# Performance work log

Hardware: AMD Instinct MI355X
Metric: run time of the kernel (lower is better)

## Reference

```python
import jax, jax.numpy as jnp
import numpy as np

B, T, C, H = 128, 512, 128, 64  # batch, seq, n_embd, head_size


def setup_inputs() -> dict:
    key = jax.random.key(0)
    ks = jax.random.split(key, 6)
    s = 1.0 / np.sqrt(C)
    return {
        "x": jax.random.normal(ks[0], (B, T, C), dtype=jnp.float32),
        "Wg": jax.random.normal(ks[1], (C, C), dtype=jnp.float32) * s,
        "bg": jnp.zeros((C,), dtype=jnp.float32),
        "Wk": jax.random.normal(ks[2], (C, H), dtype=jnp.float32) * s,
        "Wq": jax.random.normal(ks[3], (C, H), dtype=jnp.float32) * s,
        "Wv": jax.random.normal(ks[4], (C, H), dtype=jnp.float32) * s,
    }


def reference(x, Wg, bg, Wk, Wq, Wv):
    # GateLayer: x * sigmoid(Linear(x))
    g = jax.nn.sigmoid(jnp.einsum('btc,cd->btd', x, Wg) + bg)
    xg = x * g
    k = jnp.einsum('btc,ch->bth', xg, Wk)
    q = jnp.einsum('btc,ch->bth', xg, Wq)
    v = jnp.einsum('btc,ch->bth', xg, Wv)
    # NOTE: original scales by C**-0.5 (n_embd), not head_size**-0.5
    scale = C ** -0.5
    wei = jnp.einsum('bqh,bkh->bqk', q, k) * scale  # [B,T,T]
    causal = jnp.tril(jnp.ones((T, T), dtype=bool))
    wei = jnp.where(causal, wei, -jnp.inf)
    wei = jax.nn.softmax(wei, axis=-1)
    # dropout is identity in eval mode
    out = jnp.einsum('bqk,bkh->bqh', wei, v)  # [B,T,H]
    return out
```

## Files before the change

### kernel.cpp

```cpp
#include <hip/hip_runtime.h>


#define BB 128
#define TB 512
#define CC 128
#define HH 64

static constexpr float SCALE = 0.088388347648318447f;

typedef __attribute__((ext_vector_type(8))) short bf16x8;
typedef __attribute__((ext_vector_type(8))) unsigned short u16x8;
typedef __attribute__((ext_vector_type(4))) float f32x4;

__device__ inline unsigned short f2bf(float f) {
    union { float f; unsigned u; } x; x.f = f;
    unsigned r = x.u + 0x7fff + ((x.u >> 16) & 1);
    return (unsigned short)(r >> 16);
}
__device__ inline float bf2f(unsigned short h) {
    union { unsigned u; float f; } x; x.u = ((unsigned)h) << 16;
    return x.f;
}
__device__ inline bf16x8 pack8(float4 a, float4 b) {
    bf16x8 o;
    o[0] = (short)f2bf(a.x); o[1] = (short)f2bf(a.y);
    o[2] = (short)f2bf(a.z); o[3] = (short)f2bf(a.w);
    o[4] = (short)f2bf(b.x); o[5] = (short)f2bf(b.y);
    o[6] = (short)f2bf(b.z); o[7] = (short)f2bf(b.w);
    return o;
}

__global__ void prep_weights(const float* __restrict__ Wg, const float* __restrict__ Wk,
                             const float* __restrict__ Wq, const float* __restrict__ Wv,
                             unsigned short* __restrict__ WgT, unsigned short* __restrict__ WkT,
                             unsigned short* __restrict__ WqT, unsigned short* __restrict__ WvT)
{
    int idx = blockIdx.x * 256 + threadIdx.x;
    if (idx < 16384) {
        int n = idx >> 7, k = idx & 127;
        WgT[idx] = f2bf(Wg[k * CC + n]);
    } else {
        int j = idx - 16384;
        int mtx = j >> 13;
        int r = j & 8191;
        int n = r >> 7, k = r & 127;
        const float* W = (mtx == 0) ? Wk : (mtx == 1) ? Wq : Wv;
        unsigned short* WT = (mtx == 0) ? WkT : (mtx == 1) ? WqT : WvT;
        WT[r] = f2bf(W[k * HH + n]);
    }
}

__global__ __launch_bounds__(256, 2) void gate_qkv_kernel(
    const float* __restrict__ x, const float* __restrict__ bg,
    const unsigned short* __restrict__ WgT, const unsigned short* __restrict__ WkT,
    const unsigned short* __restrict__ WqT, const unsigned short* __restrict__ WvT,
    unsigned short* __restrict__ qo, unsigned short* __restrict__ ko,
    unsigned short* __restrict__ vto)
{
    __shared__ unsigned short wlds[192 * 136];
    __shared__ unsigned short slice[4][32 * 40];

    const int tid  = threadIdx.x;
    const int wv   = tid >> 6;
    const int lane = tid & 63;
    const int l15  = lane & 15;
    const int quad = lane >> 4;
    const int R0   = blockIdx.x * 128;
    const int row0 = R0 + 32 * wv;

#pragma unroll
    for (int it = 0; it < 8; ++it) {
        int idx = tid + 256 * it;
        int r = idx >> 4, c8 = idx & 15;
        *(u16x8*)(wlds + r * 136 + c8 * 8) = *(const u16x8*)(WgT + r * 128 + c8 * 8);
    }

    bf16x8 bx[2][4];
#pragma unroll
    for (int mt = 0; mt < 2; ++mt)
#pragma unroll
        for (int kc = 0; kc < 4; ++kc) {
            const float* p = x + (size_t)(row0 + 16 * mt + l15) * CC + kc * 32 + quad * 8;
            float4 a = *(const float4*)p;
            float4 c = *(const float4*)(p + 4);
            bx[mt][kc] = pack8(a, c);
        }

    float4 xe[8][2];
#pragma unroll
    for (int nt = 0; nt < 8; ++nt)
#pragma unroll
        for (int mt = 0; mt < 2; ++mt)
            xe[nt][mt] = *(const float4*)(x + (size_t)(row0 + 16 * mt + l15) * CC +
                                          16 * nt + 4 * quad);

    __syncthreads();

    f32x4 acc[8][2];
#pragma unroll
    for (int nt = 0; nt < 8; ++nt)
#pragma unroll
        for (int mt = 0; mt < 2; ++mt) acc[nt][mt] = (f32x4){0.f, 0.f, 0.f, 0.f};

#pragma unroll
    for (int nt = 0; nt < 8; ++nt) {
#pragma unroll
        for (int kc = 0; kc < 4; ++kc) {
            bf16x8 aw = *(const bf16x8*)(wlds + (16 * nt + l15) * 136 + kc * 32 + quad * 8);
#pragma unroll
            for (int mt = 0; mt < 2; ++mt)
                acc[nt][mt] = __builtin_amdgcn_mfma_f32_16x16x32_bf16(
                    aw, bx[mt][kc], acc[nt][mt], 0, 0, 0);
        }
    }

    unsigned short* sl = slice[wv];
    bf16x8 bxg[2][4];
#pragma unroll
    for (int kc = 0; kc < 4; ++kc) {
#pragma unroll
        for (int half = 0; half < 2; ++half) {
            int nt = 2 * kc + half;
            float4 bgv = *(const float4*)(bg + 16 * nt + 4 * quad);
#pragma unroll
            for (int mt = 0; mt < 2; ++mt) {
                float e0 = __expf(-(acc[nt][mt][0] + bgv.x));
                float e1 = __expf(-(acc[nt][mt][1] + bgv.y));
                float e2 = __expf(-(acc[nt][mt][2] + bgv.z));
                float e3 = __expf(-(acc[nt][mt][3] + bgv.w));
                ushort4 o;
                o.x = f2bf(xe[nt][mt].x * __builtin_amdgcn_rcpf(1.f + e0));
                o.y = f2bf(xe[nt][mt].y * __builtin_amdgcn_rcpf(1.f + e1));
                o.z = f2bf(xe[nt][mt].z * __builtin_amdgcn_rcpf(1.f + e2));
                o.w = f2bf(xe[nt][mt].w * __builtin_amdgcn_rcpf(1.f + e3));
                *(ushort4*)(sl + (16 * mt + l15) * 40 + 16 * half + 4 * quad) = o;
            }
        }
#pragma unroll
        for (int mt = 0; mt < 2; ++mt)
            bxg[mt][kc] = *(const bf16x8*)(sl + (16 * mt + l15) * 40 + quad * 8);
    }

    __syncthreads();

#pragma unroll
    for (int it = 0; it < 12; ++it) {
        int idx = tid + 256 * it;
        int r = idx >> 4, c8 = idx & 15;
        const unsigned short* src = (r < 64) ? (WkT + r * 128)
                                  : (r < 128) ? (WqT + (r - 64) * 128)
                                              : (WvT + (r - 128) * 128);
        *(u16x8*)(wlds + r * 136 + c8 * 8) = *(const u16x8*)(src + c8 * 8);
    }
    __syncthreads();

    const int b = R0 >> 9, t0 = R0 & 511;
#pragma unroll
    for (int pj = 0; pj < 3; ++pj) {
        f32x4 pacc[4][2];
#pragma unroll
        for (int nt = 0; nt < 4; ++nt)
#pragma unroll
            for (int mt = 0; mt < 2; ++mt) pacc[nt][mt] = (f32x4){0.f, 0.f, 0.f, 0.f};

#pragma unroll
        for (int nt = 0; nt < 4; ++nt) {
#pragma unroll
            for (int kc = 0; kc < 4; ++kc) {
                bf16x8 aw = *(const bf16x8*)(wlds + (64 * pj + 16 * nt + l15) * 136 +
                                             kc * 32 + quad * 8);
#pragma unroll
                for (int mt = 0; mt < 2; ++mt)
                    pacc[nt][mt] = __builtin_amdgcn_mfma_f32_16x16x32_bf16(
                        aw, bxg[mt][kc], pacc[nt][mt], 0, 0, 0);
            }
        }

        if (pj < 2) {
            unsigned short* O = (pj == 0) ? ko : qo;
#pragma unroll
            for (int nt = 0; nt < 4; ++nt)
#pragma unroll
                for (int mt = 0; mt < 2; ++mt) {
                    int m = 32 * wv + 16 * mt + l15;
                    ushort4 h;
                    h.x = f2bf(pacc[nt][mt][0]); h.y = f2bf(pacc[nt][mt][1]);
                    h.z = f2bf(pacc[nt][mt][2]); h.w = f2bf(pacc[nt][mt][3]);
                    *(ushort4*)(O + (size_t)(R0 + m) * HH + 16 * nt + quad * 4) = h;
                }
        } else {
#pragma unroll
            for (int nt = 0; nt < 4; ++nt)
#pragma unroll
                for (int mt = 0; mt < 2; ++mt) {
                    int m = 32 * wv + 16 * mt + l15;
                    unsigned short* dst =
                        vto + (size_t)b * (HH * TB) + (16 * nt + quad * 4) * TB + t0 + m;
#pragma unroll
                    for (int r = 0; r < 4; ++r)
                        dst[r * TB] = f2bf(pacc[nt][mt][r]);
                }
        }
    }
}

__device__ __forceinline__ void pv_nomax(const f32x4* s, f32x4& lacc, f32x4* o4,
                                         unsigned short* ps, const bf16x8* bv0,
                                         const bf16x8* bv1, const bf16x8 ones,
                                         int wave, int l15, int quad)
{
#pragma unroll
    for (int nt = 0; nt < 4; ++nt)
#pragma unroll
        for (int r = 0; r < 4; ++r)
            ps[(16 * wave + quad * 4 + r) * 76 + 16 * nt + l15] = f2bf(__expf(s[nt][r]));

    bf16x8 ap0 = *(const bf16x8*)(ps + (16 * wave + l15) * 76 + quad * 8);
    bf16x8 ap1 = *(const bf16x8*)(ps + (16 * wave + l15) * 76 + 32 + quad * 8);
    lacc = __builtin_amdgcn_mfma_f32_16x16x32_bf16(ap0, ones, lacc, 0, 0, 0);
    lacc = __builtin_amdgcn_mfma_f32_16x16x32_bf16(ap1, ones, lacc, 0, 0, 0);
#pragma unroll
    for (int nt = 0; nt < 4; ++nt) {
        o4[nt] = __builtin_amdgcn_mfma_f32_16x16x32_bf16(ap0, bv0[nt], o4[nt], 0, 0, 0);
        o4[nt] = __builtin_amdgcn_mfma_f32_16x16x32_bf16(ap1, bv1[nt], o4[nt], 0, 0, 0);
    }
}

__device__ __forceinline__ void attn_epilogue(const f32x4* o4, const f32x4 lacc,
                                              float* out, size_t base, int q0,
                                              int wave, int l15, int quad)
{
    float inv[4];
#pragma unroll
    for (int r = 0; r < 4; ++r) inv[r] = __builtin_amdgcn_rcpf(lacc[r]);
#pragma unroll
    for (int nt = 0; nt < 4; ++nt)
#pragma unroll
        for (int r = 0; r < 4; ++r)
            out[base + (size_t)(q0 + 16 * wave + quad * 4 + r) * HH + 16 * nt + l15] =
                o4[nt][r] * inv[r];
}

__global__ __launch_bounds__(256, 2) void attn_kernel(
    const unsigned short* __restrict__ q, const unsigned short* __restrict__ k,
    const unsigned short* __restrict__ vt, float* __restrict__ out)
{
    __shared__ unsigned short ks[64 * 72];
    __shared__ unsigned short vs[64 * 72];
    __shared__ unsigned short ps[64 * 76];

    const int tid  = threadIdx.x;
    const int wave = tid >> 6;
    const int lane = tid & 63;
    const int l15  = lane & 15;
    const int quad = lane >> 4;
    const int pr   = blockIdx.x;
    const int b    = blockIdx.y;
    const size_t base = (size_t)b * TB * HH;

    const int qtA = pr, qtB = 7 - pr;
    const int q0A = qtA * 64, q0B = qtB * 64;

    bf16x8 ones;
#pragma unroll
    for (int i = 0; i < 8; ++i) ones[i] = (short)0x3F80;

    const int r0 = tid >> 3, c8 = (tid & 7) * 8;
    const int r1 = r0 + 32;

    bf16x8 kr0 = *(const bf16x8*)(k + base + (size_t)r0 * HH + c8);
    bf16x8 kr1 = *(const bf16x8*)(k + base + (size_t)r1 * HH + c8);
    bf16x8 vr0 = *(const bf16x8*)(vt + base + (size_t)r0 * TB + c8);
    bf16x8 vr1 = *(const bf16x8*)(vt + base + (size_t)r1 * TB + c8);

    const unsigned short* qrA = q + base + (size_t)(q0A + 16 * wave + l15) * HH;
    const unsigned short* qrB = q + base + (size_t)(q0B + 16 * wave + l15) * HH;
    bf16x8 aqA0 = *(const bf16x8*)(qrA + quad * 8);
    bf16x8 aqA1 = *(const bf16x8*)(qrA + 32 + quad * 8);
    bf16x8 aqB0 = *(const bf16x8*)(qrB + quad * 8);
    bf16x8 aqB1 = *(const bf16x8*)(qrB + 32 + quad * 8);

    f32x4 oA[4], oB[4], lAacc, lBacc;
#pragma unroll
    for (int nt = 0; nt < 4; ++nt) {
        oA[nt] = (f32x4){0.f, 0.f, 0.f, 0.f};
        oB[nt] = (f32x4){0.f, 0.f, 0.f, 0.f};
    }
    lAacc = (f32x4){0.f, 0.f, 0.f, 0.f};
    lBacc = (f32x4){0.f, 0.f, 0.f, 0.f};

    const int nIt = qtB + 1;
    for (int kt = 0; kt < nIt; ++kt) {
        __syncthreads();
        *(bf16x8*)(ks + r0 * 72 + c8) = kr0;
        *(bf16x8*)(ks + r1 * 72 + c8) = kr1;
        *(bf16x8*)(vs + r0 * 72 + c8) = vr0;
        *(bf16x8*)(vs + r1 * 72 + c8) = vr1;
        __syncthreads();

        if (kt + 1 < nIt) {
            const int k0n = (kt + 1) * 64;
            kr0 = *(const bf16x8*)(k + base + (size_t)(k0n + r0) * HH + c8);
            kr1 = *(const bf16x8*)(k + base + (size_t)(k0n + r1) * HH + c8);
            vr0 = *(const bf16x8*)(vt + base + (size_t)r0 * TB + k0n + c8);
            vr1 = *(const bf16x8*)(vt + base + (size_t)r1 * TB + k0n + c8);
        }

        bf16x8 bk0[4], bk1[4], bv0[4], bv1[4];
#pragma unroll
        for (int nt = 0; nt < 4; ++nt) {
            bk0[nt] = *(const bf16x8*)(ks + (16 * nt + l15) * 72 + quad * 8);
            bk1[nt] = *(const bf16x8*)(ks + (16 * nt + l15) * 72 + 32 + quad * 8);
            bv0[nt] = *(const bf16x8*)(vs + (16 * nt + l15) * 72 + quad * 8);
            bv1[nt] = *(const bf16x8*)(vs + (16 * nt + l15) * 72 + 32 + quad * 8);
        }

        const bool actA = (kt <= qtA);

        f32x4 sA[4], sB[4];
#pragma unroll
        for (int nt = 0; nt < 4; ++nt) {
            f32x4 zb = (f32x4){0.f, 0.f, 0.f, 0.f};
            zb = __builtin_amdgcn_mfma_f32_16x16x32_bf16(aqB0, bk0[nt], zb, 0, 0, 0);
            zb = __builtin_amdgcn_mfma_f32_16x16x32_bf16(aqB1, bk1[nt], zb, 0, 0, 0);
            sB[nt] = zb;
            if (actA) {
                f32x4 za = (f32x4){0.f, 0.f, 0.f, 0.f};
                za = __builtin_amdgcn_mfma_f32_16x16x32_bf16(aqA0, bk0[nt], za, 0, 0, 0);
                za = __builtin_amdgcn_mfma_f32_16x16x32_bf16(aqA1, bk1[nt], za, 0, 0, 0);
                sA[nt] = za;
            }
        }

        if (actA) {
            const bool diagA = (kt == qtA);
#pragma unroll
            for (int nt = 0; nt < 4; ++nt)
#pragma unroll
                for (int r = 0; r < 4; ++r) {
                    float sv = sA[nt][r] * SCALE;
                    if (diagA && (16 * nt + l15) > (16 * wave + quad * 4 + r)) sv = -1e30f;
                    sA[nt][r] = sv;
                }
            pv_nomax(sA, lAacc, oA, ps, bv0, bv1, ones, wave, l15, quad);
            if (diagA) attn_epilogue(oA, lAacc, out, base, q0A, wave, l15, quad);
        }

        {
            const bool diagB = (kt == qtB);
#pragma unroll
            for (int nt = 0; nt < 4; ++nt)
#pragma unroll
                for (int r = 0; r < 4; ++r) {
                    float sv = sB[nt][r] * SCALE;
                    if (diagB && (16 * nt + l15) > (16 * wave + quad * 4 + r)) sv = -1e30f;
                    sB[nt][r] = sv;
                }
            pv_nomax(sB, lBacc, oB, ps, bv0, bv1, ones, wave, l15, quad);
        }
    }

    attn_epilogue(oB, lBacc, out, base, q0B, wave, l15, quad);
}

extern "C" void kernel_launch(void* const* d_in, const int* in_sizes, int n_in,
                              void* d_out, int out_size, void* d_ws, size_t ws_size,
                              hipStream_t stream) {
    const float* x  = (const float*)d_in[0];
    const float* Wg = (const float*)d_in[1];
    const float* bg = (const float*)d_in[2];
    const float* Wk = (const float*)d_in[3];
    const float* Wq = (const float*)d_in[4];
    const float* Wv = (const float*)d_in[5];
    float* out = (float*)d_out;

    unsigned short* ws = (unsigned short*)d_ws;
    const size_t BTH = (size_t)BB * TB * HH;
    unsigned short* qo  = ws;
    unsigned short* ko  = ws + BTH;
    unsigned short* vto = ws + 2 * BTH;
    unsigned short* WgT = ws + 3 * BTH;
    unsigned short* WkT = WgT + 16384;
    unsigned short* WqT = WkT + 8192;
    unsigned short* WvT = WqT + 8192;

    hipLaunchKernelGGL(prep_weights, dim3(160), dim3(256), 0, stream,
                       Wg, Wk, Wq, Wv, WgT, WkT, WqT, WvT);
    hipLaunchKernelGGL(gate_qkv_kernel, dim3(BB * TB / 128), dim3(256), 0, stream,
                       x, bg, WgT, WkT, WqT, WvT, qo, ko, vto);
    hipLaunchKernelGGL(attn_kernel, dim3(4, BB), dim3(256), 0, stream,
                       qo, ko, vto, out);
}
```

Measured before the change: 120.8 us.

## Split paired query tiles into one block per tile with transposed score MFMA

Each attention block previously handled two query tiles (qt and 7-qt) to balance causal work. Now each block handles a single query tile, the grid becomes (B, 8) with the longest tiles scheduled first, and launch bounds allow three blocks per CU. The score MFMA operands are swapped so each lane holds a row of P and can write four contiguous bf16 values, and exp is computed with exp2f using a pre-multiplied log2e scale. This trades the per-block load balancing for more blocks and occupancy, and the K/V tiles that were shared between the two query tiles are now reloaded by separate blocks.

```diff
diff --git a/kernel.cpp b/kernel.cpp
--- a/kernel.cpp
+++ b/kernel.cpp
@@ -6,7 +6,8 @@
 #define CC 128
 #define HH 64
 
-static constexpr float SCALE = 0.088388347648318447f;
+static constexpr float SEXP2 =
+    (float)(0.088388347648318447 * 1.4426950408889634);
 
 typedef __attribute__((ext_vector_type(8))) short bf16x8;
 typedef __attribute__((ext_vector_type(8))) unsigned short u16x8;
@@ -16,10 +17,6 @@
     union { float f; unsigned u; } x; x.f = f;
     unsigned r = x.u + 0x7fff + ((x.u >> 16) & 1);
     return (unsigned short)(r >> 16);
-}
-__device__ inline float bf2f(unsigned short h) {
-    union { unsigned u; float f; } x; x.u = ((unsigned)h) << 16;
-    return x.f;
 }
 __device__ inline bf16x8 pack8(float4 a, float4 b) {
     bf16x8 o;
@@ -204,44 +201,7 @@
     }
 }
 
-__device__ __forceinline__ void pv_nomax(const f32x4* s, f32x4& lacc, f32x4* o4,
-                                         unsigned short* ps, const bf16x8* bv0,
-                                         const bf16x8* bv1, const bf16x8 ones,
-                                         int wave, int l15, int quad)
-{
-#pragma unroll
-    for (int nt = 0; nt < 4; ++nt)
-#pragma unroll
-        for (int r = 0; r < 4; ++r)
-            ps[(16 * wave + quad * 4 + r) * 76 + 16 * nt + l15] = f2bf(__expf(s[nt][r]));
-
-    bf16x8 ap0 = *(const bf16x8*)(ps + (16 * wave + l15) * 76 + quad * 8);
-    bf16x8 ap1 = *(const bf16x8*)(ps + (16 * wave + l15) * 76 + 32 + quad * 8);
-    lacc = __builtin_amdgcn_mfma_f32_16x16x32_bf16(ap0, ones, lacc, 0, 0, 0);
-    lacc = __builtin_amdgcn_mfma_f32_16x16x32_bf16(ap1, ones, lacc, 0, 0, 0);
-#pragma unroll
-    for (int nt = 0; nt < 4; ++nt) {
-        o4[nt] = __builtin_amdgcn_mfma_f32_16x16x32_bf16(ap0, bv0[nt], o4[nt], 0, 0, 0);
-        o4[nt] = __builtin_amdgcn_mfma_f32_16x16x32_bf16(ap1, bv1[nt], o4[nt], 0, 0, 0);
-    }
-}
-
-__device__ __forceinline__ void attn_epilogue(const f32x4* o4, const f32x4 lacc,
-                                              float* out, size_t base, int q0,
-                                              int wave, int l15, int quad)
-{
-    float inv[4];
-#pragma unroll
-    for (int r = 0; r < 4; ++r) inv[r] = __builtin_amdgcn_rcpf(lacc[r]);
-#pragma unroll
-    for (int nt = 0; nt < 4; ++nt)
-#pragma unroll
-        for (int r = 0; r < 4; ++r)
-            out[base + (size_t)(q0 + 16 * wave + quad * 4 + r) * HH + 16 * nt + l15] =
-                o4[nt][r] * inv[r];
-}
-
-__global__ __launch_bounds__(256, 2) void attn_kernel(
+__global__ __launch_bounds__(256, 3) void attn_kernel(
     const unsigned short* __restrict__ q, const unsigned short* __restrict__ k,
     const unsigned short* __restrict__ vt, float* __restrict__ out)
 {
@@ -254,12 +214,10 @@
     const int lane = tid & 63;
     const int l15  = lane & 15;
     const int quad = lane >> 4;
-    const int pr   = blockIdx.x;
-    const int b    = blockIdx.y;
+    const int b    = blockIdx.x;
+    const int qt   = 7 - blockIdx.y;
+    const int q0   = qt * 64;
     const size_t base = (size_t)b * TB * HH;
-
-    const int qtA = pr, qtB = 7 - pr;
-    const int q0A = qtA * 64, q0B = qtB * 64;
 
     bf16x8 ones;
 #pragma unroll
@@ -273,23 +231,16 @@
     bf16x8 vr0 = *(const bf16x8*)(vt + base + (size_t)r0 * TB + c8);
     bf16x8 vr1 = *(const bf16x8*)(vt + base + (size_t)r1 * TB + c8);
 
-    const unsigned short* qrA = q + base + (size_t)(q0A + 16 * wave + l15) * HH;
-    const unsigned short* qrB = q + base + (size_t)(q0B + 16 * wave + l15) * HH;
-    bf16x8 aqA0 = *(const bf16x8*)(qrA + quad * 8);
-    bf16x8 aqA1 = *(const bf16x8*)(qrA + 32 + quad * 8);
-    bf16x8 aqB0 = *(const bf16x8*)(qrB + quad * 8);
-    bf16x8 aqB1 = *(const bf16x8*)(qrB + 32 + quad * 8);
-
-    f32x4 oA[4], oB[4], lAacc, lBacc;
-#pragma unroll
-    for (int nt = 0; nt < 4; ++nt) {
-        oA[nt] = (f32x4){0.f, 0.f, 0.f, 0.f};
-        oB[nt] = (f32x4){0.f, 0.f, 0.f, 0.f};
-    }
-    lAacc = (f32x4){0.f, 0.f, 0.f, 0.f};
-    lBacc = (f32x4){0.f, 0.f, 0.f, 0.f};
-
-    const int nIt = qtB + 1;
+    const unsigned short* qr = q + base + (size_t)(q0 + 16 * wave + l15) * HH;
+    bf16x8 aq0 = *(const bf16x8*)(qr + quad * 8);
+    bf16x8 aq1 = *(const bf16x8*)(qr + 32 + quad * 8);
+
+    f32x4 o[4], lacc;
+#pragma unroll
+    for (int nt = 0; nt < 4; ++nt) o[nt] = (f32x4){0.f, 0.f, 0.f, 0.f};
+    lacc = (f32x4){0.f, 0.f, 0.f, 0.f};
+
+    const int nIt = qt + 1;
     for (int kt = 0; kt < nIt; ++kt) {
         __syncthreads();
         *(bf16x8*)(ks + r0 * 72 + c8) = kr0;
@@ -315,52 +266,51 @@
             bv1[nt] = *(const bf16x8*)(vs + (16 * nt + l15) * 72 + 32 + quad * 8);
         }
 
-        const bool actA = (kt <= qtA);
-
-        f32x4 sA[4], sB[4];
-#pragma unroll
-        for (int nt = 0; nt < 4; ++nt) {
-            f32x4 zb = (f32x4){0.f, 0.f, 0.f, 0.f};
-            zb = __builtin_amdgcn_mfma_f32_16x16x32_bf16(aqB0, bk0[nt], zb, 0, 0, 0);
-            zb = __builtin_amdgcn_mfma_f32_16x16x32_bf16(aqB1, bk1[nt], zb, 0, 0, 0);
-            sB[nt] = zb;
-            if (actA) {
-                f32x4 za = (f32x4){0.f, 0.f, 0.f, 0.f};
-                za = __builtin_amdgcn_mfma_f32_16x16x32_bf16(aqA0, bk0[nt], za, 0, 0, 0);
-                za = __builtin_amdgcn_mfma_f32_16x16x32_bf16(aqA1, bk1[nt], za, 0, 0, 0);
-                sA[nt] = za;
+        f32x4 s[4];
+#pragma unroll
+        for (int nt = 0; nt < 4; ++nt) {
+            f32x4 z = (f32x4){0.f, 0.f, 0.f, 0.f};
+            z = __builtin_amdgcn_mfma_f32_16x16x32_bf16(bk0[nt], aq0, z, 0, 0, 0);
+            z = __builtin_amdgcn_mfma_f32_16x16x32_bf16(bk1[nt], aq1, z, 0, 0, 0);
+            s[nt] = z;
+        }
+
+        const bool diag = (kt == qt);
+        unsigned short* pr = ps + (16 * wave + l15) * 76;
+#pragma unroll
+        for (int nt = 0; nt < 4; ++nt) {
+            float p[4];
+#pragma unroll
+            for (int r = 0; r < 4; ++r) {
+                float sv = s[nt][r] * SEXP2;
+                if (diag && (16 * nt + 4 * quad + r) > (16 * wave + l15)) sv = -1e30f;
+                p[r] = exp2f(sv);
             }
-        }
-
-        if (actA) {
-            const bool diagA = (kt == qtA);
-#pragma unroll
-            for (int nt = 0; nt < 4; ++nt)
-#pragma unroll
-                for (int r = 0; r < 4; ++r) {
-                    float sv = sA[nt][r] * SCALE;
-                    if (diagA && (16 * nt + l15) > (16 * wave + quad * 4 + r)) sv = -1e30f;
-                    sA[nt][r] = sv;
-                }
-            pv_nomax(sA, lAacc, oA, ps, bv0, bv1, ones, wave, l15, quad);
-            if (diagA) attn_epilogue(oA, lAacc, out, base, q0A, wave, l15, quad);
-        }
-
-        {
-            const bool diagB = (kt == qtB);
-#pragma unroll
-            for (int nt = 0; nt < 4; ++nt)
-#pragma unroll
-                for (int r = 0; r < 4; ++r) {
-                    float sv = sB[nt][r] * SCALE;
-                    if (diagB && (16 * nt + l15) > (16 * wave + quad * 4 + r)) sv = -1e30f;
-                    sB[nt][r] = sv;
-                }
-            pv_nomax(sB, lBacc, oB, ps, bv0, bv1, ones, wave, l15, quad);
-        }
-    }
-
-    attn_epilogue(oB, lBacc, out, base, q0B, wave, l15, quad);
+            ushort4 h;
+            h.x = f2bf(p[0]); h.y = f2bf(p[1]); h.z = f2bf(p[2]); h.w = f2bf(p[3]);
+            *(ushort4*)(pr + 16 * nt + 4 * quad) = h;
+        }
+
+        bf16x8 ap0 = *(const bf16x8*)(pr + quad * 8);
+        bf16x8 ap1 = *(const bf16x8*)(pr + 32 + quad * 8);
+        lacc = __builtin_amdgcn_mfma_f32_16x16x32_bf16(ap0, ones, lacc, 0, 0, 0);
+        lacc = __builtin_amdgcn_mfma_f32_16x16x32_bf16(ap1, ones, lacc, 0, 0, 0);
+#pragma unroll
+        for (int nt = 0; nt < 4; ++nt) {
+            o[nt] = __builtin_amdgcn_mfma_f32_16x16x32_bf16(ap0, bv0[nt], o[nt], 0, 0, 0);
+            o[nt] = __builtin_amdgcn_mfma_f32_16x16x32_bf16(ap1, bv1[nt], o[nt], 0, 0, 0);
+        }
+    }
+
+    float inv[4];
+#pragma unroll
+    for (int r = 0; r < 4; ++r) inv[r] = __builtin_amdgcn_rcpf(lacc[r]);
+#pragma unroll
+    for (int nt = 0; nt < 4; ++nt)
+#pragma unroll
+        for (int r = 0; r < 4; ++r)
+            out[base + (size_t)(q0 + 16 * wave + quad * 4 + r) * HH + 16 * nt + l15] =
+                o[nt][r] * inv[r];
 }
 
 extern "C" void kernel_launch(void* const* d_in, const int* in_sizes, int n_in,
@@ -388,6 +338,6 @@
                        Wg, Wk, Wq, Wv, WgT, WkT, WqT, WvT);
     hipLaunchKernelGGL(gate_qkv_kernel, dim3(BB * TB / 128), dim3(256), 0, stream,
                        x, bg, WgT, WkT, WqT, WvT, qo, ko, vto);
-    hipLaunchKernelGGL(attn_kernel, dim3(4, BB), dim3(256), 0, stream,
+    hipLaunchKernelGGL(attn_kernel, dim3(BB, 8), dim3(256), 0, stream,
                        qo, ko, vto, out);
 }
```

After: 116.8 us. 3.3% less time.
